# Optimization experiments

Measured on AMD Instinct MI355X. Metric: run time of the kernel, lower is better.

The kernel has to match this reference:

```python
import jax, jax.numpy as jnp
import numpy as np

B, S, K, N = 4, 2048, 4096, 4096

def setup_inputs() -> dict:
    key = jax.random.key(0)
    k1, k2, k3, k4 = jax.random.split(key, 4)
    # int8 quantized activations and weight (stored as int8, matmul accumulates int32)
    a = jax.random.randint(k1, (B, S, K), -128, 128, dtype=jnp.int32).astype(jnp.int8)
    w = jax.random.randint(k3, (K, N), -128, 128, dtype=jnp.int32).astype(jnp.int8)
    # dequant scales: per-token for activations, per-output-channel for weight
    a_s = (jax.random.uniform(k2, (B, S, 1), dtype=jnp.float32) + 0.5) * 0.01
    w_s = (jax.random.uniform(k4, (1, N), dtype=jnp.float32) + 0.5) * 0.01
    return {"a": a, "a_s": a_s, "w": w, "w_s": w_s}

def reference(a, a_s, w, w_s):
    # torch._int_mm loop with padding), fused with dequant epilogue.
    acc = jnp.einsum('bsk,kn->bsn', a, w, preferred_element_type=jnp.int32)
    # dequant: float32 accum * input_scale * weight_scale, cast to model dtype (fp16)
    out = (acc.astype(jnp.float32) * a_s * w_s).astype(jnp.float16)
    return out
```

## Files before the change

kernel.cpp:

```cpp
#include <hip/hip_runtime.h>
#include <cstdint>
#include <cstddef>


#define M_DIM 8192
#define N_DIM 4096
#define K_DIM 4096

#define PACKA_BLOCKS ((M_DIM * K_DIM / 4) / 256)
#define TRANS_BLOCKS ((N_DIM / 64) * (K_DIM / 64))

typedef int v4i  __attribute__((ext_vector_type(4)));
typedef int v16i __attribute__((ext_vector_type(16)));

__device__ __forceinline__ uint32_t pack4(int x, int y, int z, int w)
{
    return (uint32_t)(x & 0xff) | ((uint32_t)(y & 0xff) << 8) |
           ((uint32_t)(z & 0xff) << 16) | ((uint32_t)(w & 0xff) << 24);
}

__global__ void __launch_bounds__(256) prepare_kernel(
    const int* __restrict__ a, const int* __restrict__ w,
    uint8_t* __restrict__ pa, uint8_t* __restrict__ wt)
{
    __shared__ int lds[64][65];

    if (blockIdx.x < PACKA_BLOCKS) {
        const size_t idx = (size_t)blockIdx.x * 256 + threadIdx.x;
        int4 x = ((const int4*)a)[idx];
        ((uint32_t*)pa)[idx] = pack4(x.x, x.y, x.z, x.w);
        return;
    }

    const int tile = blockIdx.x - PACKA_BLOCKS;
    const int t  = threadIdx.x;
    const int n0 = (tile & 63) * 64;
    const int k0 = (tile >> 6) * 64;

#pragma unroll
    for (int i = 0; i < 4; ++i) {
        int v   = t + 256 * i;
        int row = v >> 4;
        int cq  = v & 15;
        int4 x = *(const int4*)(w + (size_t)(k0 + row) * N_DIM + n0 + cq * 4);
        lds[row][cq * 4 + 0] = x.x;
        lds[row][cq * 4 + 1] = x.y;
        lds[row][cq * 4 + 2] = x.z;
        lds[row][cq * 4 + 3] = x.w;
    }
    __syncthreads();

    const int n_local = t >> 2;
    const int c       = t & 3;
    uint32_t o[4];
#pragma unroll
    for (int j = 0; j < 4; ++j)
        o[j] = pack4(lds[c * 16 + j * 4 + 0][n_local],
                     lds[c * 16 + j * 4 + 1][n_local],
                     lds[c * 16 + j * 4 + 2][n_local],
                     lds[c * 16 + j * 4 + 3][n_local]);
    *(uint4*)(wt + (size_t)(n0 + n_local) * K_DIM + k0 + c * 16) =
        make_uint4(o[0], o[1], o[2], o[3]);
}

__device__ __forceinline__ void async_copy16(const void* gptr, void* lptr)
{
    __builtin_amdgcn_global_load_lds(
        (const __attribute__((address_space(1))) uint32_t*)gptr,
        (__attribute__((address_space(3))) uint32_t*)lptr,
        16, 0, 0);
}

__global__ void __launch_bounds__(256) int8_gemm_kernel(
    const uint8_t* __restrict__ A,
    const uint8_t* __restrict__ Wt,
    const float*   __restrict__ a_s,
    const float*   __restrict__ w_s,
    float*         __restrict__ out)
{
    __shared__ __align__(16) uint8_t sA[128 * 128];
    __shared__ __align__(16) uint8_t sB[128 * 128];

    const int tid   = threadIdx.x;
    const int wave  = tid >> 6;
    const int lane  = tid & 63;
    const int waveM = wave >> 1;
    const int waveN = wave & 1;

    const int bm = blockIdx.x & 63;
    const int bn = blockIdx.x >> 6;
    const int m0 = bm * 128;
    const int n0 = bn * 128;

    v16i acc[2][2];
#pragma unroll
    for (int i = 0; i < 2; ++i)
#pragma unroll
        for (int j = 0; j < 2; ++j)
#pragma unroll
            for (int r = 0; r < 16; ++r)
                acc[i][j][r] = 0;

    const int sr = lane >> 3;
    const int sc = lane & 7;

    const int frow = lane & 31;
    const int fk   = lane >> 5;

    for (int kt = 0; kt < K_DIM / 128; ++kt) {
        const int k0 = kt * 128;
#pragma unroll
        for (int s = 0; s < 4; ++s) {
            const int region = wave * 4 + s;
            const int r      = region * 8 + sr;
            const int g      = sc ^ (r & 7);
            async_copy16(A  + (size_t)(m0 + r) * K_DIM + k0 + g * 16,
                         &sA[region * 1024]);
            async_copy16(Wt + (size_t)(n0 + r) * K_DIM + k0 + g * 16,
                         &sB[region * 1024]);
        }
        __syncthreads();

#pragma unroll
        for (int s = 0; s < 4; ++s) {
            const int gc = s * 2 + fk;
            v4i af[2], bf[2];
#pragma unroll
            for (int t = 0; t < 2; ++t) {
                const int mr = waveM * 64 + t * 32 + frow;
                af[t] = *(const v4i*)(sA + mr * 128 + ((gc ^ (mr & 7)) << 4));
                const int nr = waveN * 64 + t * 32 + frow;
                bf[t] = *(const v4i*)(sB + nr * 128 + ((gc ^ (nr & 7)) << 4));
            }
#pragma unroll
            for (int mt = 0; mt < 2; ++mt)
#pragma unroll
                for (int nt = 0; nt < 2; ++nt)
                    acc[mt][nt] = __builtin_amdgcn_mfma_i32_32x32x32_i8(
                        af[mt], bf[nt], acc[mt][nt], 0, 0, 0);
        }
        __syncthreads();
    }

    const int col   = lane & 31;
    const int rbase = (lane >> 5) * 4;

#pragma unroll
    for (int mt = 0; mt < 2; ++mt) {
        const int mrow0 = m0 + waveM * 64 + mt * 32 + rbase;
        float asv[16];
#pragma unroll
        for (int reg = 0; reg < 16; ++reg)
            asv[reg] = a_s[mrow0 + (reg & 3) + 8 * (reg >> 2)];
#pragma unroll
        for (int nt = 0; nt < 2; ++nt) {
            const int n = n0 + waveN * 64 + nt * 32 + col;
            const float wsv = w_s[n];
#pragma unroll
            for (int reg = 0; reg < 16; ++reg) {
                const int row = mrow0 + (reg & 3) + 8 * (reg >> 2);
                float v = (float)acc[mt][nt][reg] * asv[reg] * wsv;
                v = (float)(_Float16)v;
                out[(size_t)row * N_DIM + n] = v;
            }
        }
    }
}

extern "C" void kernel_launch(void* const* d_in, const int* in_sizes, int n_in,
                              void* d_out, int out_size, void* d_ws, size_t ws_size,
                              hipStream_t stream)
{
    const int*   a   = (const int*)  d_in[0];
    const float* a_s = (const float*)d_in[1];
    const int*   w   = (const int*)  d_in[2];
    const float* w_s = (const float*)d_in[3];
    float*       out = (float*)d_out;

    uint8_t* wt = (uint8_t*)d_ws;
    uint8_t* pa = (uint8_t*)d_ws + (size_t)N_DIM * K_DIM;

    prepare_kernel<<<PACKA_BLOCKS + TRANS_BLOCKS, 256, 0, stream>>>(a, w, pa, wt);

    int8_gemm_kernel<<<(M_DIM / 128) * (N_DIM / 128), 256, 0, stream>>>(
        pa, wt, a_s, w_s, out);
}
```

Measured before the change: 420.9 us.

## Use 256x256 tiles with 8 waves and double-buffered async LDS pipeline

Grows the GEMM block tile from 128x128 to 256x256 with 512 threads. Global-to-LDS async copies now run into double buffers split into two K halves, and explicit vmcnt waits plus raw barriers let loads of the next tile overlap MFMA work on the current one. MFMA sections are wrapped in setprio. The 128 KB of shared memory and the larger accumulator set may cut occupancy, and the fragile vmcnt accounting risks races if the count of in-flight copies is off.

```diff
diff --git a/kernel.cpp b/kernel.cpp
--- a/kernel.cpp
+++ b/kernel.cpp
@@ -71,83 +71,129 @@
         16, 0, 0);
 }
 
-__global__ void __launch_bounds__(256) int8_gemm_kernel(
+#define VMCNT4() asm volatile("s_waitcnt vmcnt(4)" ::: "memory")
+#define VMCNT0() asm volatile("s_waitcnt vmcnt(0)" ::: "memory")
+
+__global__ void __launch_bounds__(512, 2) int8_gemm_kernel(
     const uint8_t* __restrict__ A,
     const uint8_t* __restrict__ Wt,
     const float*   __restrict__ a_s,
     const float*   __restrict__ w_s,
     float*         __restrict__ out)
 {
-    __shared__ __align__(16) uint8_t sA[128 * 128];
-    __shared__ __align__(16) uint8_t sB[128 * 128];
+    __shared__ __align__(16) uint8_t sA[2][2][256 * 64];
+    __shared__ __align__(16) uint8_t sB[2][2][256 * 64];
 
     const int tid   = threadIdx.x;
     const int wave  = tid >> 6;
     const int lane  = tid & 63;
-    const int waveM = wave >> 1;
-    const int waveN = wave & 1;
-
-    const int bm = blockIdx.x & 63;
-    const int bn = blockIdx.x >> 6;
-    const int m0 = bm * 128;
-    const int n0 = bn * 128;
-
-    v16i acc[2][2];
-#pragma unroll
-    for (int i = 0; i < 2; ++i)
+    const int waveM = wave >> 2;
+    const int waveN = wave & 3;
+
+    const int bm = blockIdx.x & 31;
+    const int bn = blockIdx.x >> 5;
+    const int m0 = bm * 256;
+    const int n0 = bn * 256;
+
+    v16i acc[4][2];
+#pragma unroll
+    for (int i = 0; i < 4; ++i)
 #pragma unroll
         for (int j = 0; j < 2; ++j)
 #pragma unroll
             for (int r = 0; r < 16; ++r)
                 acc[i][j][r] = 0;
 
-    const int sr = lane >> 3;
-    const int sc = lane & 7;
+    auto stageA = [&](int buf, int kh, int kt) {
+#pragma unroll
+        for (int l = 0; l < 2; ++l) {
+            const int region = l * 8 + wave;
+            const int i      = region * 64 + lane;
+            const int row    = i >> 2;
+            const int g      = (i & 3) ^ ((row >> 1) & 3);
+            async_copy16(A + (size_t)(m0 + row) * K_DIM + kt * 128 + kh * 64 + g * 16,
+                         &sA[buf][kh][region * 1024]);
+        }
+    };
+    auto stageB = [&](int buf, int kh, int kt) {
+#pragma unroll
+        for (int l = 0; l < 2; ++l) {
+            const int region = l * 8 + wave;
+            const int i      = region * 64 + lane;
+            const int row    = i >> 2;
+            const int g      = (i & 3) ^ ((row >> 1) & 3);
+            async_copy16(Wt + (size_t)(n0 + row) * K_DIM + kt * 128 + kh * 64 + g * 16,
+                         &sB[buf][kh][region * 1024]);
+        }
+    };
 
     const int frow = lane & 31;
     const int fk   = lane >> 5;
 
-    for (int kt = 0; kt < K_DIM / 128; ++kt) {
-        const int k0 = kt * 128;
-#pragma unroll
-        for (int s = 0; s < 4; ++s) {
-            const int region = wave * 4 + s;
-            const int r      = region * 8 + sr;
-            const int g      = sc ^ (r & 7);
-            async_copy16(A  + (size_t)(m0 + r) * K_DIM + k0 + g * 16,
-                         &sA[region * 1024]);
-            async_copy16(Wt + (size_t)(n0 + r) * K_DIM + k0 + g * 16,
-                         &sB[region * 1024]);
-        }
-        __syncthreads();
-
-#pragma unroll
-        for (int s = 0; s < 4; ++s) {
-            const int gc = s * 2 + fk;
-            v4i af[2], bf[2];
-#pragma unroll
-            for (int t = 0; t < 2; ++t) {
-                const int mr = waveM * 64 + t * 32 + frow;
-                af[t] = *(const v4i*)(sA + mr * 128 + ((gc ^ (mr & 7)) << 4));
-                const int nr = waveN * 64 + t * 32 + frow;
-                bf[t] = *(const v4i*)(sB + nr * 128 + ((gc ^ (nr & 7)) << 4));
-            }
-#pragma unroll
-            for (int mt = 0; mt < 2; ++mt)
-#pragma unroll
-                for (int nt = 0; nt < 2; ++nt)
-                    acc[mt][nt] = __builtin_amdgcn_mfma_i32_32x32x32_i8(
-                        af[mt], bf[nt], acc[mt][nt], 0, 0, 0);
-        }
-        __syncthreads();
+    auto compute_kstep = [&](int buf, int s) {
+        const int kh = s >> 1;
+        const int c  = (s & 1) * 2 + fk;
+        v4i af[4], bf[2];
+#pragma unroll
+        for (int mt = 0; mt < 4; ++mt) {
+            const int ra = waveM * 128 + mt * 32 + frow;
+            af[mt] = *(const v4i*)(&sA[buf][kh][ra * 64 + ((c ^ ((ra >> 1) & 3)) << 4)]);
+        }
+#pragma unroll
+        for (int nt = 0; nt < 2; ++nt) {
+            const int rb = waveN * 64 + nt * 32 + frow;
+            bf[nt] = *(const v4i*)(&sB[buf][kh][rb * 64 + ((c ^ ((rb >> 1) & 3)) << 4)]);
+        }
+        __builtin_amdgcn_s_setprio(1);
+#pragma unroll
+        for (int mt = 0; mt < 4; ++mt)
+#pragma unroll
+            for (int nt = 0; nt < 2; ++nt)
+                acc[mt][nt] = __builtin_amdgcn_mfma_i32_32x32x32_i8(
+                    af[mt], bf[nt], acc[mt][nt], 0, 0, 0);
+        __builtin_amdgcn_s_setprio(0);
+    };
+
+    const int NT = K_DIM / 128;
+
+    stageA(0, 0, 0);
+    stageB(0, 0, 0);
+    stageA(0, 1, 0);
+    stageB(0, 1, 0);
+    VMCNT4();
+    __builtin_amdgcn_s_barrier();
+
+    for (int kt = 0; kt < NT - 1; ++kt) {
+        const int b = kt & 1;
+        stageA(b ^ 1, 0, kt + 1);
+        compute_kstep(b, 0);
+        stageB(b ^ 1, 0, kt + 1);
+        compute_kstep(b, 1);
+        VMCNT4();
+        __builtin_amdgcn_s_barrier();
+        stageA(b ^ 1, 1, kt + 1);
+        compute_kstep(b, 2);
+        stageB(b ^ 1, 1, kt + 1);
+        compute_kstep(b, 3);
+        VMCNT4();
+        __builtin_amdgcn_s_barrier();
+    }
+    {
+        const int b = (NT - 1) & 1;
+        compute_kstep(b, 0);
+        compute_kstep(b, 1);
+        VMCNT0();
+        __builtin_amdgcn_s_barrier();
+        compute_kstep(b, 2);
+        compute_kstep(b, 3);
     }
 
     const int col   = lane & 31;
     const int rbase = (lane >> 5) * 4;
 
 #pragma unroll
-    for (int mt = 0; mt < 2; ++mt) {
-        const int mrow0 = m0 + waveM * 64 + mt * 32 + rbase;
+    for (int mt = 0; mt < 4; ++mt) {
+        const int mrow0 = m0 + waveM * 128 + mt * 32 + rbase;
         float asv[16];
 #pragma unroll
         for (int reg = 0; reg < 16; ++reg)
@@ -182,6 +228,6 @@
 
     prepare_kernel<<<PACKA_BLOCKS + TRANS_BLOCKS, 256, 0, stream>>>(a, w, pa, wt);
 
-    int8_gemm_kernel<<<(M_DIM / 128) * (N_DIM / 128), 256, 0, stream>>>(
+    int8_gemm_kernel<<<(M_DIM / 256) * (N_DIM / 256), 512, 0, stream>>>(
         pa, wt, a_s, w_s, out);
 }
```

New measurement: 422.3 us. No clear change (+0.3%).
